# Performance work log

Measured on AMD Instinct MI355X. Metric: run time of the kernel, lower is better.

The kernel has to match this reference:

```python
import jax, jax.numpy as jnp
import numpy as np

NUM_FIELDS = 40
EMBED = 64
# pair indices (i<j) matching itertools.combinations order
_I, _J = np.triu_indices(NUM_FIELDS, k=1)
NUM_PAIRS = _I.shape[0]  # 780


def setup_inputs() -> dict:
    key = jax.random.key(0)
    k1, k2 = jax.random.split(key)
    feature_emb = jax.random.normal(k1, (2048, NUM_FIELDS, EMBED), dtype=jnp.float32)
    bound = 1.0 / np.sqrt(EMBED)  # nn.Linear default init range
    W = jax.random.uniform(k2, (NUM_PAIRS, EMBED, EMBED), dtype=jnp.float32,
                           minval=-bound, maxval=bound)
    return {"feature_emb": feature_emb, "W": W}


def reference(feature_emb, W):
    # field_interaction: for pair p=(i,j): (v_i @ W_p^T) * v_j
    idx_i = jnp.asarray(_I)
    idx_j = jnp.asarray(_J)
    vi = feature_emb[:, idx_i, :]  # [B, P, E]
    vj = feature_emb[:, idx_j, :]  # [B, P, E]
    # nn.Linear: y = x @ W^T  -> einsum over input-feature axis e
    out = jnp.einsum('bpe,pfe->bpf', vi, W) * vj  # [B, P, E]
    return out
```

## Files before the change

kernel.cpp:

```cpp
#include <hip/hip_runtime.h>

#define NUM_FIELDS 40
#define NPAIRS     780
#define EMBED      64
#define BATCH      2048
#define BB         64
#define PT         12
#define NBC        (BATCH/BB)
#define NPC        (NPAIRS/PT)
#define NBLK       (NBC*NPC)

#define NW_ELEMS   (NPAIRS*EMBED*EMBED)
#define NE_ELEMS   (BATCH*NUM_FIELDS*EMBED)
#define NW8        (NW_ELEMS/8)
#define NE8        (NE_ELEMS/8)

typedef __attribute__((ext_vector_type(8))) short bf16x8;
typedef __attribute__((ext_vector_type(4))) short short4v;
typedef __attribute__((ext_vector_type(4))) float f32x4;

__device__ __forceinline__ short f2bf(float f) {
    unsigned u = __builtin_bit_cast(unsigned, f);
    u += 0x7FFFu + ((u >> 16) & 1u);
    return (short)(u >> 16);
}

__global__ __launch_bounds__(256)
void cvt_all_bf16(const float* __restrict__ W, const float* __restrict__ emb,
                  short* __restrict__ dst) {
    const int total = NW8 + NE8;
    for (int i = blockIdx.x * 256 + threadIdx.x; i < total; i += gridDim.x * 256) {
        const float* src = (i < NW8) ? (W + (size_t)i * 8)
                                     : (emb + ((size_t)(i - NW8)) * 8);
        float4 a = ((const float4*)src)[0];
        float4 b = ((const float4*)src)[1];
        short4v lo, hi;
        lo.x = f2bf(a.x); lo.y = f2bf(a.y); lo.z = f2bf(a.z); lo.w = f2bf(a.w);
        hi.x = f2bf(b.x); hi.y = f2bf(b.y); hi.z = f2bf(b.z); hi.w = f2bf(b.w);
        ((short4v*)dst)[2 * (size_t)i]     = lo;
        ((short4v*)dst)[2 * (size_t)i + 1] = hi;
    }
}

__global__ __launch_bounds__(256, 5)
void bilinear_direct3(const short* __restrict__ Wbf,
                      const short* __restrict__ embbf,
                      const float* __restrict__ emb,
                      float* __restrict__ out) {
    __shared__ __align__(16) float TR[4][16][64];

    const int bid  = blockIdx.x;
    const int orig = (bid & 7) * (NBLK / 8) + (bid >> 3);
    const int bc   = orig % NBC;
    const int pc   = orig / NBC;
    const int bblk = bc * BB;
    const int p0   = pc * PT;

    const int t   = threadIdx.x;
    const int w   = t >> 6;
    const int l   = t & 63;
    const int l15 = l & 15;
    const int l4  = l >> 4;
    const int rl  = l >> 4;

    int fi = 0, rem = p0, cnt = NUM_FIELDS - 1;
    while (rem >= cnt) { rem -= cnt; --cnt; ++fi; }
    int fj = fi + 1 + rem;

    const int    bg     = bblk + 16 * w + l15;
    const float* vjbase = emb + (size_t)bg * NUM_FIELDS * EMBED;
    const short* vibase = embbf + (size_t)bg * NUM_FIELDS * EMBED + l4 * 8;

    bf16x8 bfr[2];
    {
        const short* vib = vibase + (size_t)fi * EMBED;
        bfr[0] = *(const bf16x8*)(vib);
        bfr[1] = *(const bf16x8*)(vib + 32);
    }

    const short* wb = Wbf + (size_t)p0 * (EMBED * EMBED) + l15 * EMBED + l4 * 8;

    #pragma unroll 2
    for (int pi = 0; pi < PT; ++pi) {
        const int p = p0 + pi;
        const short* wp = wb + (size_t)pi * (EMBED * EMBED);

        bf16x8 afr[8];
        #pragma unroll
        for (int nt = 0; nt < 4; ++nt) {
            afr[2 * nt]     = *(const bf16x8*)(wp + nt * 16 * EMBED);
            afr[2 * nt + 1] = *(const bf16x8*)(wp + nt * 16 * EMBED + 32);
        }

        const float* vjrow = vjbase + (size_t)fj * EMBED;
        float4 vj4[4];
        #pragma unroll
        for (int nt = 0; nt < 4; ++nt)
            vj4[nt] = *(const float4*)(vjrow + nt * 16 + l4 * 4);

        f32x4 acc[4];
        #pragma unroll
        for (int nt = 0; nt < 4; ++nt) {
            acc[nt].x = 0.f; acc[nt].y = 0.f; acc[nt].z = 0.f; acc[nt].w = 0.f;
            acc[nt] = __builtin_amdgcn_mfma_f32_16x16x32_bf16(afr[2 * nt],     bfr[0], acc[nt], 0, 0, 0);
            acc[nt] = __builtin_amdgcn_mfma_f32_16x16x32_bf16(afr[2 * nt + 1], bfr[1], acc[nt], 0, 0, 0);
        }

        {
            float* myrow = &TR[w][l15][0];
            #pragma unroll
            for (int nt = 0; nt < 4; ++nt) {
                const int slot = (nt * 4 + l4) ^ (l15 & 7);
                f32x4 o;
                o.x = acc[nt].x * vj4[nt].x;
                o.y = acc[nt].y * vj4[nt].y;
                o.z = acc[nt].z * vj4[nt].z;
                o.w = acc[nt].w * vj4[nt].w;
                *(f32x4*)(myrow + slot * 4) = o;
            }
        }

        #pragma unroll
        for (int k = 0; k < 4; ++k) {
            const int row  = 4 * k + rl;
            const int slot = l15 ^ (row & 7);
            f32x4 v = *(const f32x4*)&TR[w][row][slot * 4];
            float* dstp = out + ((size_t)(bblk + 16 * w + row) * NPAIRS + p) * EMBED
                              + l15 * 4;
            __builtin_nontemporal_store(v, (f32x4*)dstp);
        }

        int fi_n = fi, fj_n = fj + 1;
        if (fj_n == NUM_FIELDS) { fi_n = fi + 1; fj_n = fi_n + 1; }
        if (fi_n != fi) {
            const short* vib = vibase + (size_t)fi_n * EMBED;
            bfr[0] = *(const bf16x8*)(vib);
            bfr[1] = *(const bf16x8*)(vib + 32);
        }
        fi = fi_n; fj = fj_n;
    }
}

__global__ __launch_bounds__(256, 4)
void bilinear_mfma2(const float* __restrict__ emb,
                    const float* __restrict__ Wg,
                    float* __restrict__ out) {
    __shared__ __align__(16) short WbS[2][64][8][8];
    __shared__ __align__(16) short VIS[64][8][8];

    const int FBPT = 26;
    const int FNPC = NPAIRS / FBPT;
    const int FNBLK = NBC * FNPC;
    const int bid  = blockIdx.x;
    const int orig = (bid & 7) * (FNBLK / 8) + (bid >> 3);
    const int bc   = orig % NBC;
    const int pc   = orig / NBC;
    const int bblk = bc * BB;
    const int p0   = pc * FBPT;
    const int t = threadIdx.x;

    int fi = 0, rem = p0, cnt = NUM_FIELDS - 1;
    while (rem >= cnt) { rem -= cnt; --cnt; ++fi; }
    int fj = fi + 1 + rem;

    {
        const float4* Wp = (const float4*)(Wg + (size_t)p0 * EMBED * EMBED);
        #pragma unroll
        for (int k = 0; k < 4; ++k) {
            int n = t + 256 * k;
            int row = n >> 4, e4 = n & 15;
            float4 wv = Wp[n];
            float4 vv = *(const float4*)(emb +
                          ((size_t)(bblk + row) * NUM_FIELDS + fi) * EMBED + e4 * 4);
            int o = e4 >> 1, half = e4 & 1;
            int slot = o ^ (row & 7);
            short4v cw, cv;
            cw.x = f2bf(wv.x); cw.y = f2bf(wv.y); cw.z = f2bf(wv.z); cw.w = f2bf(wv.w);
            cv.x = f2bf(vv.x); cv.y = f2bf(vv.y); cv.z = f2bf(vv.z); cv.w = f2bf(vv.w);
            *(short4v*)&WbS[0][row][slot][half * 4] = cw;
            *(short4v*)&VIS[row][slot][half * 4] = cv;
        }
    }
    __syncthreads();

    const int w = t >> 6, l = t & 63, l15 = l & 15, l4 = l >> 4;
    const size_t bg = (size_t)(bblk + 16 * w + l15);
    const float* vjbase = emb + bg * NUM_FIELDS * EMBED;
    float*       obase  = out + (bg * NPAIRS) * (size_t)EMBED;

    for (int pi = 0; pi < FBPT; ++pi) {
        const int cur = pi & 1, nxt = cur ^ 1;
        const int p   = p0 + pi;
        int fi_n = fi, fj_n = fj + 1;
        if (fj_n == NUM_FIELDS) { fi_n = fi + 1; fj_n = fi_n + 1; }
        const bool havenext  = (pi + 1 < FBPT);
        const bool fi_change = havenext && (fi_n != fi);

        float4 Wpre[4], Vpre[4];
        if (havenext) {
            const float4* Wp = (const float4*)(Wg + (size_t)(p + 1) * EMBED * EMBED);
            #pragma unroll
            for (int k = 0; k < 4; ++k) Wpre[k] = Wp[t + 256 * k];
        }
        if (fi_change) {
            #pragma unroll
            for (int k = 0; k < 4; ++k) {
                int n = t + 256 * k;
                int row = n >> 4, e4 = n & 15;
                Vpre[k] = *(const float4*)(emb +
                            ((size_t)(bblk + row) * NUM_FIELDS + fi_n) * EMBED + e4 * 4);
            }
        }

        const float* vjrow = vjbase + (size_t)fj * EMBED;
        float4 vj4[4];
        #pragma unroll
        for (int nt = 0; nt < 4; ++nt)
            vj4[nt] = *(const float4*)(vjrow + nt * 16 + l4 * 4);

        bf16x8 bfr[2];
        #pragma unroll
        for (int kk = 0; kk < 2; ++kk) {
            int row  = 16 * w + l15;
            int slot = (kk * 4 + l4) ^ (row & 7);
            bfr[kk] = *(const bf16x8*)&VIS[row][slot][0];
        }

        f32x4 acc[4];
        #pragma unroll
        for (int nt = 0; nt < 4; ++nt) {
            acc[nt].x = 0.f; acc[nt].y = 0.f; acc[nt].z = 0.f; acc[nt].w = 0.f;
            #pragma unroll
            for (int kk = 0; kk < 2; ++kk) {
                int row  = 16 * nt + l15;
                int slot = (kk * 4 + l4) ^ (row & 7);
                bf16x8 afr = *(const bf16x8*)&WbS[cur][row][slot][0];
                acc[nt] = __builtin_amdgcn_mfma_f32_16x16x32_bf16(afr, bfr[kk], acc[nt], 0, 0, 0);
            }
        }

        float* orow = obase + (size_t)p * EMBED;
        #pragma unroll
        for (int nt = 0; nt < 4; ++nt) {
            f32x4 o;
            o.x = acc[nt].x * vj4[nt].x;
            o.y = acc[nt].y * vj4[nt].y;
            o.z = acc[nt].z * vj4[nt].z;
            o.w = acc[nt].w * vj4[nt].w;
            __builtin_nontemporal_store(o, (f32x4*)(orow + nt * 16 + l4 * 4));
        }

        if (havenext) {
            #pragma unroll
            for (int k = 0; k < 4; ++k) {
                int n = t + 256 * k;
                int row = n >> 4, e4 = n & 15;
                int o = e4 >> 1, half = e4 & 1;
                int slot = o ^ (row & 7);
                short4v cw;
                cw.x = f2bf(Wpre[k].x); cw.y = f2bf(Wpre[k].y);
                cw.z = f2bf(Wpre[k].z); cw.w = f2bf(Wpre[k].w);
                *(short4v*)&WbS[nxt][row][slot][half * 4] = cw;
            }
        }
        if (fi_change) {
            __syncthreads();
            #pragma unroll
            for (int k = 0; k < 4; ++k) {
                int n = t + 256 * k;
                int row = n >> 4, e4 = n & 15;
                int o = e4 >> 1, half = e4 & 1;
                int slot = o ^ (row & 7);
                short4v cv;
                cv.x = f2bf(Vpre[k].x); cv.y = f2bf(Vpre[k].y);
                cv.z = f2bf(Vpre[k].z); cv.w = f2bf(Vpre[k].w);
                *(short4v*)&VIS[row][slot][half * 4] = cv;
            }
        }

        fi = fi_n; fj = fj_n;
        __syncthreads();
    }
}

extern "C" void kernel_launch(void* const* d_in, const int* in_sizes, int n_in,
                              void* d_out, int out_size, void* d_ws, size_t ws_size,
                              hipStream_t stream) {
    const float* emb = (const float*)d_in[0];
    const float* W   = (const float*)d_in[1];
    float*       out = (float*)d_out;

    const size_t need = (size_t)(NW_ELEMS + NE_ELEMS) * sizeof(short);
    if (ws_size >= need) {
        short* Wbf   = (short*)d_ws;
        short* embbf = Wbf + NW_ELEMS;
        hipLaunchKernelGGL(cvt_all_bf16, dim3(2048), dim3(256), 0, stream, W, emb, Wbf);
        hipLaunchKernelGGL(bilinear_direct3, dim3(NBLK), dim3(256), 0, stream,
                           Wbf, embbf, emb, out);
    } else {
        hipLaunchKernelGGL(bilinear_mfma2, dim3(960), dim3(256), 0, stream, emb, W, out);
    }
}
```

Before: 175.2 us.

## Reuse W fragments across two batch sub-tiles and read vj as bf16

Doubles the batch tile per block to 128 rows, so each wave loads a pair's W fragments once and applies them to two 16-row batch groups, halving W traffic and halving the grid. The vj multiplier now comes from the bf16 copy of the embeddings instead of the fp32 original, which cuts load bytes but adds extra rounding error to the output. It also lowers the occupancy hint from 5 to 4 and doubles LDS staging per block. The fallback kernel is changed to hardcode its 64-row tile so it is unaffected.

```diff
diff --git a/kernel.cpp b/kernel.cpp
--- a/kernel.cpp
+++ b/kernel.cpp
@@ -4,7 +4,7 @@
 #define NPAIRS     780
 #define EMBED      64
 #define BATCH      2048
-#define BB         64
+#define BB         128
 #define PT         12
 #define NBC        (BATCH/BB)
 #define NPC        (NPAIRS/PT)
@@ -23,6 +23,9 @@
     unsigned u = __builtin_bit_cast(unsigned, f);
     u += 0x7FFFu + ((u >> 16) & 1u);
     return (short)(u >> 16);
+}
+__device__ __forceinline__ float bf2f(short h) {
+    return __builtin_bit_cast(float, (unsigned)((unsigned short)h) << 16);
 }
 
 __global__ __launch_bounds__(256)
@@ -42,12 +45,11 @@
     }
 }
 
-__global__ __launch_bounds__(256, 5)
-void bilinear_direct3(const short* __restrict__ Wbf,
+__global__ __launch_bounds__(256, 4)
+void bilinear_direct4(const short* __restrict__ Wbf,
                       const short* __restrict__ embbf,
-                      const float* __restrict__ emb,
                       float* __restrict__ out) {
-    __shared__ __align__(16) float TR[4][16][64];
+    __shared__ __align__(16) float TR[4][2][16][64];
 
     const int bid  = blockIdx.x;
     const int orig = (bid & 7) * (NBLK / 8) + (bid >> 3);
@@ -67,15 +69,18 @@
     while (rem >= cnt) { rem -= cnt; --cnt; ++fi; }
     int fj = fi + 1 + rem;
 
-    const int    bg     = bblk + 16 * w + l15;
-    const float* vjbase = emb + (size_t)bg * NUM_FIELDS * EMBED;
-    const short* vibase = embbf + (size_t)bg * NUM_FIELDS * EMBED + l4 * 8;
-
-    bf16x8 bfr[2];
+    const int r0 = bblk + 16 * w + l15;
+    const short* erow0 = embbf + (size_t)r0 * NUM_FIELDS * EMBED;
+    const short* erow1 = erow0 + (size_t)64 * NUM_FIELDS * EMBED;
+
+    bf16x8 bfr[2][2];
     {
-        const short* vib = vibase + (size_t)fi * EMBED;
-        bfr[0] = *(const bf16x8*)(vib);
-        bfr[1] = *(const bf16x8*)(vib + 32);
+        const short* v0 = erow0 + (size_t)fi * EMBED + l4 * 8;
+        const short* v1 = erow1 + (size_t)fi * EMBED + l4 * 8;
+        bfr[0][0] = *(const bf16x8*)(v0);
+        bfr[0][1] = *(const bf16x8*)(v0 + 32);
+        bfr[1][0] = *(const bf16x8*)(v1);
+        bfr[1][1] = *(const bf16x8*)(v1 + 32);
     }
 
     const short* wb = Wbf + (size_t)p0 * (EMBED * EMBED) + l15 * EMBED + l4 * 8;
@@ -92,50 +97,59 @@
             afr[2 * nt + 1] = *(const bf16x8*)(wp + nt * 16 * EMBED + 32);
         }
 
-        const float* vjrow = vjbase + (size_t)fj * EMBED;
-        float4 vj4[4];
-        #pragma unroll
-        for (int nt = 0; nt < 4; ++nt)
-            vj4[nt] = *(const float4*)(vjrow + nt * 16 + l4 * 4);
-
-        f32x4 acc[4];
-        #pragma unroll
-        for (int nt = 0; nt < 4; ++nt) {
-            acc[nt].x = 0.f; acc[nt].y = 0.f; acc[nt].z = 0.f; acc[nt].w = 0.f;
-            acc[nt] = __builtin_amdgcn_mfma_f32_16x16x32_bf16(afr[2 * nt],     bfr[0], acc[nt], 0, 0, 0);
-            acc[nt] = __builtin_amdgcn_mfma_f32_16x16x32_bf16(afr[2 * nt + 1], bfr[1], acc[nt], 0, 0, 0);
-        }
-
-        {
-            float* myrow = &TR[w][l15][0];
+        #pragma unroll
+        for (int bt = 0; bt < 2; ++bt) {
+            const short* vjrow = (bt ? erow1 : erow0) + (size_t)fj * EMBED;
+
+            short4v vjh[4];
+            #pragma unroll
+            for (int nt = 0; nt < 4; ++nt)
+                vjh[nt] = *(const short4v*)(vjrow + nt * 16 + l4 * 4);
+
+            f32x4 acc[4];
+            #pragma unroll
+            for (int nt = 0; nt < 4; ++nt) {
+                acc[nt].x = 0.f; acc[nt].y = 0.f; acc[nt].z = 0.f; acc[nt].w = 0.f;
+                acc[nt] = __builtin_amdgcn_mfma_f32_16x16x32_bf16(afr[2 * nt],     bfr[bt][0], acc[nt], 0, 0, 0);
+                acc[nt] = __builtin_amdgcn_mfma_f32_16x16x32_bf16(afr[2 * nt + 1], bfr[bt][1], acc[nt], 0, 0, 0);
+            }
+
+            float* myrow = &TR[w][bt][l15][0];
             #pragma unroll
             for (int nt = 0; nt < 4; ++nt) {
                 const int slot = (nt * 4 + l4) ^ (l15 & 7);
                 f32x4 o;
-                o.x = acc[nt].x * vj4[nt].x;
-                o.y = acc[nt].y * vj4[nt].y;
-                o.z = acc[nt].z * vj4[nt].z;
-                o.w = acc[nt].w * vj4[nt].w;
+                o.x = acc[nt].x * bf2f(vjh[nt].x);
+                o.y = acc[nt].y * bf2f(vjh[nt].y);
+                o.z = acc[nt].z * bf2f(vjh[nt].z);
+                o.w = acc[nt].w * bf2f(vjh[nt].w);
                 *(f32x4*)(myrow + slot * 4) = o;
             }
         }
 
         #pragma unroll
-        for (int k = 0; k < 4; ++k) {
-            const int row  = 4 * k + rl;
-            const int slot = l15 ^ (row & 7);
-            f32x4 v = *(const f32x4*)&TR[w][row][slot * 4];
-            float* dstp = out + ((size_t)(bblk + 16 * w + row) * NPAIRS + p) * EMBED
-                              + l15 * 4;
-            __builtin_nontemporal_store(v, (f32x4*)dstp);
+        for (int bt = 0; bt < 2; ++bt) {
+            #pragma unroll
+            for (int k = 0; k < 4; ++k) {
+                const int row  = 4 * k + rl;
+                const int slot = l15 ^ (row & 7);
+                f32x4 v = *(const f32x4*)&TR[w][bt][row][slot * 4];
+                float* dstp = out +
+                    ((size_t)(bblk + bt * 64 + 16 * w + row) * NPAIRS + p) * EMBED
+                    + l15 * 4;
+                __builtin_nontemporal_store(v, (f32x4*)dstp);
+            }
         }
 
         int fi_n = fi, fj_n = fj + 1;
         if (fj_n == NUM_FIELDS) { fi_n = fi + 1; fj_n = fi_n + 1; }
         if (fi_n != fi) {
-            const short* vib = vibase + (size_t)fi_n * EMBED;
-            bfr[0] = *(const bf16x8*)(vib);
-            bfr[1] = *(const bf16x8*)(vib + 32);
+            const short* v0 = erow0 + (size_t)fi_n * EMBED + l4 * 8;
+            const short* v1 = erow1 + (size_t)fi_n * EMBED + l4 * 8;
+            bfr[0][0] = *(const bf16x8*)(v0);
+            bfr[0][1] = *(const bf16x8*)(v0 + 32);
+            bfr[1][0] = *(const bf16x8*)(v1);
+            bfr[1][1] = *(const bf16x8*)(v1 + 32);
         }
         fi = fi_n; fj = fj_n;
     }
@@ -150,12 +164,12 @@
 
     const int FBPT = 26;
     const int FNPC = NPAIRS / FBPT;
-    const int FNBLK = NBC * FNPC;
+    const int FNBLK = (BATCH / 64) * FNPC;
     const int bid  = blockIdx.x;
     const int orig = (bid & 7) * (FNBLK / 8) + (bid >> 3);
-    const int bc   = orig % NBC;
-    const int pc   = orig / NBC;
-    const int bblk = bc * BB;
+    const int bc   = orig % (BATCH / 64);
+    const int pc   = orig / (BATCH / 64);
+    const int bblk = bc * 64;
     const int p0   = pc * FBPT;
     const int t = threadIdx.x;
 
@@ -295,8 +309,8 @@
         short* Wbf   = (short*)d_ws;
         short* embbf = Wbf + NW_ELEMS;
         hipLaunchKernelGGL(cvt_all_bf16, dim3(2048), dim3(256), 0, stream, W, emb, Wbf);
-        hipLaunchKernelGGL(bilinear_direct3, dim3(NBLK), dim3(256), 0, stream,
-                           Wbf, embbf, emb, out);
+        hipLaunchKernelGGL(bilinear_direct4, dim3(NBLK), dim3(256), 0, stream,
+                           Wbf, embbf, out);
     } else {
         hipLaunchKernelGGL(bilinear_mfma2, dim3(960), dim3(256), 0, stream, emb, W, out);
     }
```

Measured after the change: 141.7 us. -19.1%, faster.
